# Optimization experiments

Measured on AMD Instinct MI355X. Metric: run time of the kernel, lower is better.

The kernel has to match this reference:

```python
import jax, jax.numpy as jnp
import numpy as np

N = 50000      # nodes
E = 400000     # edges (before self-loops)
F_IN = 128     # input_embedding_dim
HID = 256      # hidden_dim
HEADS = 4      # gat_heads
C1 = HID // HEADS  # per-head channels layer 0
OUT = 128      # output_node_dim
G = 64         # graphs in batch
NEG_SLOPE = 0.2


def setup_inputs() -> dict:
    key = jax.random.key(0)
    ks = jax.random.split(key, 12)
    s = lambda fan: 1.0 / np.sqrt(fan)
    embedded_x = jax.random.normal(ks[0], (N, F_IN), jnp.float32)
    edge_index = jax.random.randint(ks[1], (2, E), 0, N, dtype=jnp.int32)
    batch_idx = jnp.sort(jax.random.randint(ks[2], (N,), 0, G, dtype=jnp.int32))
    # layer 0: GATConv(F_IN -> C1, heads=HEADS, concat=True)
    W1 = jax.random.normal(ks[3], (F_IN, HEADS * C1), jnp.float32) * s(F_IN)
    att_src1 = jax.random.normal(ks[4], (HEADS, C1), jnp.float32) * s(C1)
    att_dst1 = jax.random.normal(ks[5], (HEADS, C1), jnp.float32) * s(C1)
    b1 = jnp.zeros((HEADS * C1,), jnp.float32)
    # layer 1 (last): GATConv(HID -> OUT, heads=1, concat=False)
    W2 = jax.random.normal(ks[6], (HID, OUT), jnp.float32) * s(HID)
    att_src2 = jax.random.normal(ks[7], (1, OUT), jnp.float32) * s(OUT)
    att_dst2 = jax.random.normal(ks[8], (1, OUT), jnp.float32) * s(OUT)
    b2 = jnp.zeros((OUT,), jnp.float32)
    return {"embedded_x": embedded_x, "edge_index": edge_index, "batch_idx": batch_idx,
            "W1": W1, "att_src1": att_src1, "att_dst1": att_dst1, "b1": b1,
            "W2": W2, "att_src2": att_src2, "att_dst2": att_dst2, "b2": b2}


def gat_conv(x, src, dst, W, att_src, att_dst, bias, heads, out_ch, concat):
    n = x.shape[0]
    xw = (x @ W).reshape(n, heads, out_ch)              # [N,H,C]
    a_s = (xw * att_src[None]).sum(-1)                  # [N,H]
    a_d = (xw * att_dst[None]).sum(-1)                  # [N,H]
    e = jax.nn.leaky_relu(a_s[src] + a_d[dst], NEG_SLOPE)  # [E',H]
    # segment softmax over incoming edges of each dst node (self-loops guarantee non-empty)
    m = jax.ops.segment_max(e, dst, num_segments=n)
    ee = jnp.exp(e - m[dst])
    denom = jax.ops.segment_sum(ee, dst, num_segments=n)
    alpha = ee / denom[dst]                             # [E',H]
    msg = xw[src] * alpha[:, :, None]                   # [E',H,C]
    out = jax.ops.segment_sum(msg, dst, num_segments=n) # [N,H,C]
    out = out.reshape(n, heads * out_ch) if concat else out.mean(axis=1)
    return out + bias


def reference(embedded_x, edge_index, batch_idx, W1, att_src1, att_dst1, b1, W2, att_src2, att_dst2, b2):
    loops = jnp.arange(N, dtype=edge_index.dtype)
    src = jnp.concatenate([edge_index[0], loops])
    dst = jnp.concatenate([edge_index[1], loops])
    h = gat_conv(embedded_x, src, dst, W1, att_src1, att_dst1, b1, HEADS, C1, True)
    h = jax.nn.elu(h)  # dropout is identity in eval
    h = gat_conv(h, src, dst, W2, att_src2, att_dst2, b2, 1, OUT, False)
    h = jax.nn.elu(h)
    # final_node_transform is Identity (current_dim == output_node_dim)
    counts = jax.ops.segment_sum(jnp.ones((N,), h.dtype), batch_idx, num_segments=G)
    graph_embedding = jax.ops.segment_sum(h, batch_idx, num_segments=G) / jnp.maximum(counts, 1.0)[:, None]
    return (graph_embedding, h)
```

## Files before the change

kernel.cpp:

```cpp
#include <hip/hip_runtime.h>

#define NN   50000
#define NE   400000
#define NET  450000
#define NG   64
#define NEG  0.2f

using bf16x8 = __attribute__((ext_vector_type(8))) short;
using f32x4  = __attribute__((ext_vector_type(4))) float;

__device__ inline float b2f(unsigned short u){
  union{unsigned int i; float f;} v; v.i = ((unsigned int)u) << 16; return v.f;
}
__device__ inline unsigned short f2b(float f){
  union{float f; unsigned int i;} v; v.f = f;
  unsigned int r = (v.i + 0x7fffu + ((v.i >> 16) & 1u)) >> 16;
  return (unsigned short)r;
}
__device__ inline float sane(float o){
  return (o > -1e30f && o < 1e30f) ? o : 0.f;
}
__device__ inline float lrelu_clamp(float e){
  e = fmaxf(e, NEG * e);
  return fminf(e, 60.f);
}

__global__ void zero_all(int* __restrict__ deg, float* __restrict__ pools, int* __restrict__ cnt){
  int i = blockIdx.x * 256 + threadIdx.x;
  if (i < NN) deg[i] = 0;
  if (i < NG * 128) pools[i] = 0.f;
  if (i < NG) cnt[i] = 0;
}

__device__ inline void pack_one(const float* W, unsigned short* Bp, int t, int K, int N){
  int nk = K / 32;
  int lane = t & 63; int rest = t >> 6;
  int kit = rest % nk; int nt = rest / nk;
  int quad = lane >> 4, n = lane & 15;
  unsigned short* dst = Bp + (size_t)t * 8;
#pragma unroll
  for (int j = 0; j < 8; j++)
    dst[j] = f2b(W[(size_t)(kit*32 + quad*8 + j) * N + nt*16 + n]);
}
__global__ void pack_both(const float* __restrict__ W1, const float* __restrict__ W2,
                          unsigned short* __restrict__ Bp1, unsigned short* __restrict__ Bp2){
  int t = blockIdx.x * 256 + threadIdx.x;
  if (t < 4096) pack_one(W1, Bp1, t, 128, 256);
  else          pack_one(W2, Bp2, t - 4096, 256, 128);
}

__global__ void gemm1_fused(const float* __restrict__ X, const unsigned short* __restrict__ Bp,
                            const float* __restrict__ av, const float* __restrict__ dv,
                            unsigned short* __restrict__ C,
                            float* __restrict__ a_s, float* __restrict__ a_d){
  constexpr int NK = 4, NT = 16;
  int lane = threadIdx.x & 63, wave = threadIdx.x >> 6;
  int mbase = (blockIdx.x * 4 + wave) * 16;
  if (mbase >= NN) return;
  int quad = lane >> 4, nn = lane & 15;
  int arow = mbase + nn; if (arow >= NN) arow = NN - 1;
  const float* Xr = X + (size_t)arow * 128 + quad * 8;
  bf16x8 afrag[NK];
#pragma unroll
  for (int kit = 0; kit < NK; kit++){
    bf16x8 a;
#pragma unroll
    for (int j = 0; j < 8; j++) a[j] = (short)f2b(Xr[kit * 32 + j]);
    afrag[kit] = a;
  }
  float sd0=0,sd1=0,sd2=0,sd3=0, dd0=0,dd1=0,dd2=0,dd3=0;
#pragma unroll
  for (int nt = 0; nt < NT; nt++){
    f32x4 acc = {0.f, 0.f, 0.f, 0.f};
#pragma unroll
    for (int kit = 0; kit < NK; kit++){
      bf16x8 bfrag = *(const bf16x8*)(Bp + ((size_t)(nt*NK + kit) * 64 + lane) * 8);
      acc = __builtin_amdgcn_mfma_f32_16x16x32_bf16(afrag[kit], bfrag, acc, 0, 0, 0);
    }
    int col = nt * 16 + nn;
    float avc = av[col], dvc = dv[col];
    sd0 += acc[0]*avc; dd0 += acc[0]*dvc;
    sd1 += acc[1]*avc; dd1 += acc[1]*dvc;
    sd2 += acc[2]*avc; dd2 += acc[2]*dvc;
    sd3 += acc[3]*avc; dd3 += acc[3]*dvc;
#pragma unroll
    for (int r = 0; r < 4; r++){
      int row = mbase + quad * 4 + r;
      if (row < NN) C[(size_t)row * 256 + col] = f2b(acc[r]);
    }
    if ((nt & 3) == 3){
      int hh = nt >> 2;
#pragma unroll
      for (int off = 1; off < 16; off <<= 1){
        sd0 += __shfl_xor(sd0, off); sd1 += __shfl_xor(sd1, off);
        sd2 += __shfl_xor(sd2, off); sd3 += __shfl_xor(sd3, off);
        dd0 += __shfl_xor(dd0, off); dd1 += __shfl_xor(dd1, off);
        dd2 += __shfl_xor(dd2, off); dd3 += __shfl_xor(dd3, off);
      }
      if (nn == 0){
        int row = mbase + quad * 4;
        if (row + 0 < NN){ a_s[(row+0)*4+hh] = sd0; a_d[(row+0)*4+hh] = dd0; }
        if (row + 1 < NN){ a_s[(row+1)*4+hh] = sd1; a_d[(row+1)*4+hh] = dd1; }
        if (row + 2 < NN){ a_s[(row+2)*4+hh] = sd2; a_d[(row+2)*4+hh] = dd2; }
        if (row + 3 < NN){ a_s[(row+3)*4+hh] = sd3; a_d[(row+3)*4+hh] = dd3; }
      }
      sd0=sd1=sd2=sd3=dd0=dd1=dd2=dd3=0.f;
    }
  }
}

__global__ void gemm2_fused(const unsigned short* __restrict__ A, const unsigned short* __restrict__ Bp,
                            const float* __restrict__ av, const float* __restrict__ dv,
                            unsigned short* __restrict__ C,
                            float* __restrict__ a_s, float* __restrict__ a_d){
  constexpr int NK = 8, NT = 8;
  int lane = threadIdx.x & 63, wave = threadIdx.x >> 6;
  int mbase = (blockIdx.x * 4 + wave) * 16;
  if (mbase >= NN) return;
  int quad = lane >> 4, nn = lane & 15;
  int arow = mbase + nn; if (arow >= NN) arow = NN - 1;
  const unsigned short* Ar = A + (size_t)arow * 256 + quad * 8;
  bf16x8 afrag[NK];
#pragma unroll
  for (int kit = 0; kit < NK; kit++)
    afrag[kit] = *(const bf16x8*)(Ar + kit * 32);
  float sd0=0,sd1=0,sd2=0,sd3=0, dd0=0,dd1=0,dd2=0,dd3=0;
#pragma unroll
  for (int nt = 0; nt < NT; nt++){
    f32x4 acc = {0.f, 0.f, 0.f, 0.f};
#pragma unroll
    for (int kit = 0; kit < NK; kit++){
      bf16x8 bfrag = *(const bf16x8*)(Bp + ((size_t)(nt*NK + kit) * 64 + lane) * 8);
      acc = __builtin_amdgcn_mfma_f32_16x16x32_bf16(afrag[kit], bfrag, acc, 0, 0, 0);
    }
    int col = nt * 16 + nn;
    float avc = av[col], dvc = dv[col];
    sd0 += acc[0]*avc; dd0 += acc[0]*dvc;
    sd1 += acc[1]*avc; dd1 += acc[1]*dvc;
    sd2 += acc[2]*avc; dd2 += acc[2]*dvc;
    sd3 += acc[3]*avc; dd3 += acc[3]*dvc;
#pragma unroll
    for (int r = 0; r < 4; r++){
      int row = mbase + quad * 4 + r;
      if (row < NN) C[(size_t)row * 128 + col] = f2b(acc[r]);
    }
  }
#pragma unroll
  for (int off = 1; off < 16; off <<= 1){
    sd0 += __shfl_xor(sd0, off); sd1 += __shfl_xor(sd1, off);
    sd2 += __shfl_xor(sd2, off); sd3 += __shfl_xor(sd3, off);
    dd0 += __shfl_xor(dd0, off); dd1 += __shfl_xor(dd1, off);
    dd2 += __shfl_xor(dd2, off); dd3 += __shfl_xor(dd3, off);
  }
  if (nn == 0){
    int row = mbase + quad * 4;
    if (row + 0 < NN){ a_s[row+0] = sd0; a_d[row+0] = dd0; }
    if (row + 1 < NN){ a_s[row+1] = sd1; a_d[row+1] = dd1; }
    if (row + 2 < NN){ a_s[row+2] = sd2; a_d[row+2] = dd2; }
    if (row + 3 < NN){ a_s[row+3] = sd3; a_d[row+3] = dd3; }
  }
}

__global__ void count_deg(const int* __restrict__ ei, int* __restrict__ deg){
  int t = blockIdx.x * blockDim.x + threadIdx.x;
  if (t >= NET) return;
  int d = (t < NE) ? ei[NE + t] : (t - NE);
  if (d < 0) d = 0; if (d >= NN) d = NN - 1;
  atomicAdd(&deg[d], 1);
}

__global__ void scan_block(const int* __restrict__ in, int* __restrict__ out_excl,
                           int* __restrict__ bsums, int n){
  __shared__ int s[256];
  int tid = threadIdx.x, gid = blockIdx.x * 256 + tid;
  int v = (gid < n) ? in[gid] : 0;
  s[tid] = v; __syncthreads();
  for (int off = 1; off < 256; off <<= 1){
    int t = (tid >= off) ? s[tid - off] : 0;
    __syncthreads();
    s[tid] += t;
    __syncthreads();
  }
  if (gid < n) out_excl[gid] = s[tid] - v;
  if (tid == 255) bsums[blockIdx.x] = s[255];
}

__global__ void scan_add2(int* __restrict__ offs, const int* __restrict__ bsums,
                          int* __restrict__ cursor, int n){
  __shared__ int lds[256];
  int b = blockIdx.x, tid = threadIdx.x;
  int v = 0;
  for (int i = tid; i < b; i += 256) v += bsums[i];
  lds[tid] = v; __syncthreads();
  for (int off = 128; off; off >>= 1){
    if (tid < off) lds[tid] += lds[tid + off];
    __syncthreads();
  }
  int prefix = lds[0];
  int gid = b * 256 + tid;
  if (gid < n){
    int o = offs[gid] + prefix;
    offs[gid] = o; cursor[gid] = o;
  }
  if (gid == 0) offs[n] = NET;
}

__global__ void fill_csr(const int* __restrict__ ei, int* __restrict__ cursor,
                         int* __restrict__ csr){
  int t = blockIdx.x * blockDim.x + threadIdx.x;
  if (t >= NET) return;
  int s = (t < NE) ? ei[t]      : (t - NE);
  int d = (t < NE) ? ei[NE + t] : (t - NE);
  if (d < 0) d = 0; if (d >= NN) d = NN - 1;
  int pos = atomicAdd(&cursor[d], 1);
  if (pos >= 0 && pos < NET) csr[pos] = s;
}

__global__ void agg1(const unsigned short* __restrict__ xw, const float* __restrict__ a_s,
                     const float* __restrict__ a_d, const int* __restrict__ offs,
                     const int* __restrict__ csr, const float* __restrict__ bias,
                     unsigned short* __restrict__ h1){
  int lane = threadIdx.x & 63;
  int node = (blockIdx.x * blockDim.x + threadIdx.x) >> 6;
  if (node >= NN) return;
  int h = lane >> 4;
  int beg = offs[node], end = offs[node + 1];
  if (beg < 0) beg = 0; if (end > NET) end = NET;
  float adv = a_d[node * 4 + h];
  float l0=0,l1=0,l2=0,l3=0;
  float c00=0,c01=0,c02=0,c03=0;
  float c10=0,c11=0,c12=0,c13=0;
  float c20=0,c21=0,c22=0,c23=0;
  float c30=0,c31=0,c32=0,c33=0;
  int e = beg;
  for (; e + 8 <= end; e += 8){
    int s0 = csr[e],   s1 = csr[e+1], s2 = csr[e+2], s3 = csr[e+3];
    int s4 = csr[e+4], s5 = csr[e+5], s6 = csr[e+6], s7 = csr[e+7];
    float p0 = __expf(lrelu_clamp(a_s[s0*4+h] + adv));
    float p1 = __expf(lrelu_clamp(a_s[s1*4+h] + adv));
    float p2 = __expf(lrelu_clamp(a_s[s2*4+h] + adv));
    float p3 = __expf(lrelu_clamp(a_s[s3*4+h] + adv));
    float p4 = __expf(lrelu_clamp(a_s[s4*4+h] + adv));
    float p5 = __expf(lrelu_clamp(a_s[s5*4+h] + adv));
    float p6 = __expf(lrelu_clamp(a_s[s6*4+h] + adv));
    float p7 = __expf(lrelu_clamp(a_s[s7*4+h] + adv));
    ushort4 x0 = *(const ushort4*)(xw + (size_t)s0 * 256 + lane * 4);
    ushort4 x1 = *(const ushort4*)(xw + (size_t)s1 * 256 + lane * 4);
    ushort4 x2 = *(const ushort4*)(xw + (size_t)s2 * 256 + lane * 4);
    ushort4 x3 = *(const ushort4*)(xw + (size_t)s3 * 256 + lane * 4);
    ushort4 x4 = *(const ushort4*)(xw + (size_t)s4 * 256 + lane * 4);
    ushort4 x5 = *(const ushort4*)(xw + (size_t)s5 * 256 + lane * 4);
    ushort4 x6 = *(const ushort4*)(xw + (size_t)s6 * 256 + lane * 4);
    ushort4 x7 = *(const ushort4*)(xw + (size_t)s7 * 256 + lane * 4);
    l0 += p0 + p4; l1 += p1 + p5; l2 += p2 + p6; l3 += p3 + p7;
    c00 += p0*b2f(x0.x); c01 += p0*b2f(x0.y); c02 += p0*b2f(x0.z); c03 += p0*b2f(x0.w);
    c10 += p1*b2f(x1.x); c11 += p1*b2f(x1.y); c12 += p1*b2f(x1.z); c13 += p1*b2f(x1.w);
    c20 += p2*b2f(x2.x); c21 += p2*b2f(x2.y); c22 += p2*b2f(x2.z); c23 += p2*b2f(x2.w);
    c30 += p3*b2f(x3.x); c31 += p3*b2f(x3.y); c32 += p3*b2f(x3.z); c33 += p3*b2f(x3.w);
    c00 += p4*b2f(x4.x); c01 += p4*b2f(x4.y); c02 += p4*b2f(x4.z); c03 += p4*b2f(x4.w);
    c10 += p5*b2f(x5.x); c11 += p5*b2f(x5.y); c12 += p5*b2f(x5.z); c13 += p5*b2f(x5.w);
    c20 += p6*b2f(x6.x); c21 += p6*b2f(x6.y); c22 += p6*b2f(x6.z); c23 += p6*b2f(x6.w);
    c30 += p7*b2f(x7.x); c31 += p7*b2f(x7.y); c32 += p7*b2f(x7.z); c33 += p7*b2f(x7.w);
  }
  for (; e < end; e++){
    int s0 = csr[e];
    float p0 = __expf(lrelu_clamp(a_s[s0*4+h] + adv));
    ushort4 x0 = *(const ushort4*)(xw + (size_t)s0 * 256 + lane * 4);
    l0 += p0; c00 += p0*b2f(x0.x); c01 += p0*b2f(x0.y); c02 += p0*b2f(x0.z); c03 += p0*b2f(x0.w);
  }
  float l = (l0 + l1) + (l2 + l3);
  float C0 = (c00 + c10) + (c20 + c30);
  float C1 = (c01 + c11) + (c21 + c31);
  float C2 = (c02 + c12) + (c22 + c32);
  float C3 = (c03 + c13) + (c23 + c33);
  if (!(l > 0.f)) l = 1.f;
  float inv = 1.f / l;
  float4 b4 = *(const float4*)(bias + lane * 4);
  float v; ushort4 o;
  v = C0 * inv + b4.x; v = v > 0.f ? v : expm1f(v); o.x = f2b(sane(v));
  v = C1 * inv + b4.y; v = v > 0.f ? v : expm1f(v); o.y = f2b(sane(v));
  v = C2 * inv + b4.z; v = v > 0.f ? v : expm1f(v); o.z = f2b(sane(v));
  v = C3 * inv + b4.w; v = v > 0.f ? v : expm1f(v); o.w = f2b(sane(v));
  *(ushort4*)(h1 + (size_t)node * 256 + lane * 4) = o;
}

__global__ void agg2(const unsigned short* __restrict__ xw, const float* __restrict__ a_s,
                     const float* __restrict__ a_d, const int* __restrict__ offs,
                     const int* __restrict__ csr, const float* __restrict__ bias,
                     float* __restrict__ hout){
  int lane = threadIdx.x & 63;
  int node = (blockIdx.x * blockDim.x + threadIdx.x) >> 6;
  if (node >= NN) return;
  int beg = offs[node], end = offs[node + 1];
  if (beg < 0) beg = 0; if (end > NET) end = NET;
  float adv = a_d[node];
  float l0=0,l1=0,l2=0,l3=0;
  float c00=0,c01=0, c10=0,c11=0, c20=0,c21=0, c30=0,c31=0;
  int e = beg;
  for (; e + 8 <= end; e += 8){
    int s0 = csr[e],   s1 = csr[e+1], s2 = csr[e+2], s3 = csr[e+3];
    int s4 = csr[e+4], s5 = csr[e+5], s6 = csr[e+6], s7 = csr[e+7];
    float p0 = __expf(lrelu_clamp(a_s[s0] + adv));
    float p1 = __expf(lrelu_clamp(a_s[s1] + adv));
    float p2 = __expf(lrelu_clamp(a_s[s2] + adv));
    float p3 = __expf(lrelu_clamp(a_s[s3] + adv));
    float p4 = __expf(lrelu_clamp(a_s[s4] + adv));
    float p5 = __expf(lrelu_clamp(a_s[s5] + adv));
    float p6 = __expf(lrelu_clamp(a_s[s6] + adv));
    float p7 = __expf(lrelu_clamp(a_s[s7] + adv));
    ushort2 x0 = *(const ushort2*)(xw + (size_t)s0 * 128 + lane * 2);
    ushort2 x1 = *(const ushort2*)(xw + (size_t)s1 * 128 + lane * 2);
    ushort2 x2 = *(const ushort2*)(xw + (size_t)s2 * 128 + lane * 2);
    ushort2 x3 = *(const ushort2*)(xw + (size_t)s3 * 128 + lane * 2);
    ushort2 x4 = *(const ushort2*)(xw + (size_t)s4 * 128 + lane * 2);
    ushort2 x5 = *(const ushort2*)(xw + (size_t)s5 * 128 + lane * 2);
    ushort2 x6 = *(const ushort2*)(xw + (size_t)s6 * 128 + lane * 2);
    ushort2 x7 = *(const ushort2*)(xw + (size_t)s7 * 128 + lane * 2);
    l0 += p0 + p4; l1 += p1 + p5; l2 += p2 + p6; l3 += p3 + p7;
    c00 += p0*b2f(x0.x); c01 += p0*b2f(x0.y);
    c10 += p1*b2f(x1.x); c11 += p1*b2f(x1.y);
    c20 += p2*b2f(x2.x); c21 += p2*b2f(x2.y);
    c30 += p3*b2f(x3.x); c31 += p3*b2f(x3.y);
    c00 += p4*b2f(x4.x); c01 += p4*b2f(x4.y);
    c10 += p5*b2f(x5.x); c11 += p5*b2f(x5.y);
    c20 += p6*b2f(x6.x); c21 += p6*b2f(x6.y);
    c30 += p7*b2f(x7.x); c31 += p7*b2f(x7.y);
  }
  for (; e < end; e++){
    int s0 = csr[e];
    float p0 = __expf(lrelu_clamp(a_s[s0] + adv));
    ushort2 x0 = *(const ushort2*)(xw + (size_t)s0 * 128 + lane * 2);
    l0 += p0; c00 += p0*b2f(x0.x); c01 += p0*b2f(x0.y);
  }
  float l = (l0 + l1) + (l2 + l3);
  float C0 = (c00 + c10) + (c20 + c30);
  float C1 = (c01 + c11) + (c21 + c31);
  if (!(l > 0.f)) l = 1.f;
  float inv = 1.f / l;
  float v0 = C0 * inv + bias[lane*2];   v0 = v0 > 0.f ? v0 : expm1f(v0);
  float v1 = C1 * inv + bias[lane*2+1]; v1 = v1 > 0.f ? v1 : expm1f(v1);
  float2 o; o.x = sane(v0); o.y = sane(v1);
  *(float2*)(hout + (size_t)node * 128 + lane * 2) = o;
}

__global__ void pool_kernel(const float* __restrict__ h, const int* __restrict__ batch,
                            float* __restrict__ pools, int* __restrict__ cnt){
  int c = threadIdx.x;
  int n0 = blockIdx.x * 16;
  if (n0 >= NN) return;
  int nend = n0 + 16; if (nend > NN) nend = NN;
  int cur = batch[n0];
  cur = (cur < 0) ? 0 : (cur >= NG ? NG - 1 : cur);
  float sum = 0.f; int count = 0;
  for (int n = n0; n < nend; n++){
    int g = batch[n];
    g = (g < 0) ? 0 : (g >= NG ? NG - 1 : g);
    if (g != cur){
      atomicAdd(&pools[cur * 128 + c], sum);
      if (c == 0) atomicAdd(&cnt[cur], count);
      sum = 0.f; count = 0; cur = g;
    }
    sum += h[(size_t)n * 128 + c];
    count++;
  }
  atomicAdd(&pools[cur * 128 + c], sum);
  if (c == 0) atomicAdd(&cnt[cur], count);
}

__global__ void final_kernel(const float* __restrict__ pools, const int* __restrict__ cnt,
                             float* __restrict__ out){
  int g = blockIdx.x, c = threadIdx.x;
  float d = fmaxf((float)cnt[g], 1.0f);
  out[g * 128 + c] = sane(pools[g * 128 + c] / d);
}

extern "C" void kernel_launch(void* const* d_in, const int* in_sizes, int n_in,
                              void* d_out, int out_size, void* d_ws, size_t ws_size,
                              hipStream_t stream){
  const float* x    = (const float*)d_in[0];
  const int*   ei   = (const int*)d_in[1];
  const int*   bat  = (const int*)d_in[2];
  const float* W1   = (const float*)d_in[3];
  const float* av1  = (const float*)d_in[4];
  const float* dv1  = (const float*)d_in[5];
  const float* b1   = (const float*)d_in[6];
  const float* W2   = (const float*)d_in[7];
  const float* av2  = (const float*)d_in[8];
  const float* dv2  = (const float*)d_in[9];
  const float* b2   = (const float*)d_in[10];

  char* w = (char*)d_ws;
  size_t o = 0;
  auto carve = [&](size_t bytes) -> char* {
    char* p = w + o; o += (bytes + 255) & ~(size_t)255; return p;
  };
  unsigned short* Bp1   = (unsigned short*)carve((size_t)4096 * 8 * 2);
  unsigned short* Bp2   = (unsigned short*)carve((size_t)4096 * 8 * 2);
  float*          a_s1v = (float*)carve((size_t)NN * 4 * 4);
  float*          a_d1v = (float*)carve((size_t)NN * 4 * 4);
  float*          a_s2v = (float*)carve((size_t)NN * 4);
  float*          a_d2v = (float*)carve((size_t)NN * 4);
  int*            deg   = (int*)carve((size_t)NN * 4);
  int*            offs  = (int*)carve((size_t)(NN + 1) * 4);
  int*            cursor= (int*)carve((size_t)NN * 4);
  int*            bsums = (int*)carve(256 * 4);
  int*            csr   = (int*)carve((size_t)NET * 4);
  float*          pools = (float*)carve((size_t)NG * 128 * 4);
  int*            cnt   = (int*)carve((size_t)NG * 4);
  unsigned short* xw1   = (unsigned short*)carve((size_t)NN * 256 * 2);
  unsigned short* h1b   = (unsigned short*)carve((size_t)NN * 256 * 2);
  unsigned short* xw2   = (unsigned short*)carve((size_t)NN * 128 * 2);

  float* out_ge = (float*)d_out;
  float* out_h  = (float*)d_out + NG * 128;

  zero_all<<<196, 256, 0, stream>>>(deg, pools, cnt);
  pack_both<<<32, 256, 0, stream>>>(W1, W2, Bp1, Bp2);

  count_deg<<<(NET + 255) / 256, 256, 0, stream>>>(ei, deg);
  scan_block<<<196, 256, 0, stream>>>(deg, offs, bsums, NN);
  scan_add2<<<196, 256, 0, stream>>>(offs, bsums, cursor, NN);
  fill_csr<<<(NET + 255) / 256, 256, 0, stream>>>(ei, cursor, csr);

  gemm1_fused<<<782, 256, 0, stream>>>(x, Bp1, av1, dv1, xw1, a_s1v, a_d1v);
  agg1<<<12500, 256, 0, stream>>>(xw1, a_s1v, a_d1v, offs, csr, b1, h1b);

  gemm2_fused<<<782, 256, 0, stream>>>(h1b, Bp2, av2, dv2, xw2, a_s2v, a_d2v);
  agg2<<<12500, 256, 0, stream>>>(xw2, a_s2v, a_d2v, offs, csr, b2, out_h);

  pool_kernel<<<3125, 128, 0, stream>>>(out_h, bat, pools, cnt);
  final_kernel<<<NG, 128, 0, stream>>>(pools, cnt, out_ge);
}
```

Measured before the change: 286.2 us.

## Precompute per-edge attention weights in separate edge passes before aggregation

Adds edge-parallel kernels that compute exp(leaky_relu(a_s+a_d)) once per edge and head, scattering them into CSR order using positions recorded by fill_csr. The aggregation kernels then read these weights instead of recomputing the exp for every lane, and their unroll drops from 8 to 4. The intent is to cut redundant transcendental work and scattered a_s gathers inside the wave-per-node loops. The cost is two extra launches and extra global traffic for the weight arrays, and xw2 now reuses xw1's buffer.

```diff
diff --git a/kernel.cpp b/kernel.cpp
--- a/kernel.cpp
+++ b/kernel.cpp
@@ -206,65 +206,83 @@
 }
 
 __global__ void fill_csr(const int* __restrict__ ei, int* __restrict__ cursor,
-                         int* __restrict__ csr){
+                         int* __restrict__ csr, int* __restrict__ epos){
   int t = blockIdx.x * blockDim.x + threadIdx.x;
   if (t >= NET) return;
   int s = (t < NE) ? ei[t]      : (t - NE);
   int d = (t < NE) ? ei[NE + t] : (t - NE);
   if (d < 0) d = 0; if (d >= NN) d = NN - 1;
   int pos = atomicAdd(&cursor[d], 1);
-  if (pos >= 0 && pos < NET) csr[pos] = s;
-}
-
-__global__ void agg1(const unsigned short* __restrict__ xw, const float* __restrict__ a_s,
-                     const float* __restrict__ a_d, const int* __restrict__ offs,
-                     const int* __restrict__ csr, const float* __restrict__ bias,
-                     unsigned short* __restrict__ h1){
+  if (pos < 0) pos = 0; if (pos >= NET) pos = NET - 1;
+  csr[pos] = s;
+  epos[t] = pos;
+}
+
+__global__ void epass1(const int* __restrict__ ei, const int* __restrict__ epos,
+                       const float* __restrict__ a_s, const float* __restrict__ a_d,
+                       float* __restrict__ pw){
+  int t = blockIdx.x * 256 + threadIdx.x;
+  if (t >= NET) return;
+  int s = (t < NE) ? ei[t]      : (t - NE);
+  int d = (t < NE) ? ei[NE + t] : (t - NE);
+  if (s < 0) s = 0; if (s >= NN) s = NN - 1;
+  if (d < 0) d = 0; if (d >= NN) d = NN - 1;
+  int pos = epos[t];
+  float4 as = *(const float4*)(a_s + (size_t)s * 4);
+  float4 ad = *(const float4*)(a_d + (size_t)d * 4);
+  float4 p;
+  p.x = __expf(lrelu_clamp(as.x + ad.x));
+  p.y = __expf(lrelu_clamp(as.y + ad.y));
+  p.z = __expf(lrelu_clamp(as.z + ad.z));
+  p.w = __expf(lrelu_clamp(as.w + ad.w));
+  *(float4*)(pw + (size_t)pos * 4) = p;
+}
+
+__global__ void epass2(const int* __restrict__ ei, const int* __restrict__ epos,
+                       const float* __restrict__ a_s, const float* __restrict__ a_d,
+                       float* __restrict__ pw){
+  int t = blockIdx.x * 256 + threadIdx.x;
+  if (t >= NET) return;
+  int s = (t < NE) ? ei[t]      : (t - NE);
+  int d = (t < NE) ? ei[NE + t] : (t - NE);
+  if (s < 0) s = 0; if (s >= NN) s = NN - 1;
+  if (d < 0) d = 0; if (d >= NN) d = NN - 1;
+  pw[epos[t]] = __expf(lrelu_clamp(a_s[s] + a_d[d]));
+}
+
+__global__ void agg1(const unsigned short* __restrict__ xw, const float* __restrict__ pw,
+                     const int* __restrict__ offs, const int* __restrict__ csr,
+                     const float* __restrict__ bias, unsigned short* __restrict__ h1){
   int lane = threadIdx.x & 63;
   int node = (blockIdx.x * blockDim.x + threadIdx.x) >> 6;
   if (node >= NN) return;
   int h = lane >> 4;
   int beg = offs[node], end = offs[node + 1];
   if (beg < 0) beg = 0; if (end > NET) end = NET;
-  float adv = a_d[node * 4 + h];
   float l0=0,l1=0,l2=0,l3=0;
   float c00=0,c01=0,c02=0,c03=0;
   float c10=0,c11=0,c12=0,c13=0;
   float c20=0,c21=0,c22=0,c23=0;
   float c30=0,c31=0,c32=0,c33=0;
   int e = beg;
-  for (; e + 8 <= end; e += 8){
-    int s0 = csr[e],   s1 = csr[e+1], s2 = csr[e+2], s3 = csr[e+3];
-    int s4 = csr[e+4], s5 = csr[e+5], s6 = csr[e+6], s7 = csr[e+7];
-    float p0 = __expf(lrelu_clamp(a_s[s0*4+h] + adv));
-    float p1 = __expf(lrelu_clamp(a_s[s1*4+h] + adv));
-    float p2 = __expf(lrelu_clamp(a_s[s2*4+h] + adv));
-    float p3 = __expf(lrelu_clamp(a_s[s3*4+h] + adv));
-    float p4 = __expf(lrelu_clamp(a_s[s4*4+h] + adv));
-    float p5 = __expf(lrelu_clamp(a_s[s5*4+h] + adv));
-    float p6 = __expf(lrelu_clamp(a_s[s6*4+h] + adv));
-    float p7 = __expf(lrelu_clamp(a_s[s7*4+h] + adv));
+  for (; e + 4 <= end; e += 4){
+    int s0 = csr[e], s1 = csr[e+1], s2 = csr[e+2], s3 = csr[e+3];
+    float p0 = pw[(size_t)(e+0)*4 + h];
+    float p1 = pw[(size_t)(e+1)*4 + h];
+    float p2 = pw[(size_t)(e+2)*4 + h];
+    float p3 = pw[(size_t)(e+3)*4 + h];
     ushort4 x0 = *(const ushort4*)(xw + (size_t)s0 * 256 + lane * 4);
     ushort4 x1 = *(const ushort4*)(xw + (size_t)s1 * 256 + lane * 4);
     ushort4 x2 = *(const ushort4*)(xw + (size_t)s2 * 256 + lane * 4);
     ushort4 x3 = *(const ushort4*)(xw + (size_t)s3 * 256 + lane * 4);
-    ushort4 x4 = *(const ushort4*)(xw + (size_t)s4 * 256 + lane * 4);
-    ushort4 x5 = *(const ushort4*)(xw + (size_t)s5 * 256 + lane * 4);
-    ushort4 x6 = *(const ushort4*)(xw + (size_t)s6 * 256 + lane * 4);
-    ushort4 x7 = *(const ushort4*)(xw + (size_t)s7 * 256 + lane * 4);
-    l0 += p0 + p4; l1 += p1 + p5; l2 += p2 + p6; l3 += p3 + p7;
-    c00 += p0*b2f(x0.x); c01 += p0*b2f(x0.y); c02 += p0*b2f(x0.z); c03 += p0*b2f(x0.w);
-    c10 += p1*b2f(x1.x); c11 += p1*b2f(x1.y); c12 += p1*b2f(x1.z); c13 += p1*b2f(x1.w);
-    c20 += p2*b2f(x2.x); c21 += p2*b2f(x2.y); c22 += p2*b2f(x2.z); c23 += p2*b2f(x2.w);
-    c30 += p3*b2f(x3.x); c31 += p3*b2f(x3.y); c32 += p3*b2f(x3.z); c33 += p3*b2f(x3.w);
-    c00 += p4*b2f(x4.x); c01 += p4*b2f(x4.y); c02 += p4*b2f(x4.z); c03 += p4*b2f(x4.w);
-    c10 += p5*b2f(x5.x); c11 += p5*b2f(x5.y); c12 += p5*b2f(x5.z); c13 += p5*b2f(x5.w);
-    c20 += p6*b2f(x6.x); c21 += p6*b2f(x6.y); c22 += p6*b2f(x6.z); c23 += p6*b2f(x6.w);
-    c30 += p7*b2f(x7.x); c31 += p7*b2f(x7.y); c32 += p7*b2f(x7.z); c33 += p7*b2f(x7.w);
+    l0 += p0; c00 += p0*b2f(x0.x); c01 += p0*b2f(x0.y); c02 += p0*b2f(x0.z); c03 += p0*b2f(x0.w);
+    l1 += p1; c10 += p1*b2f(x1.x); c11 += p1*b2f(x1.y); c12 += p1*b2f(x1.z); c13 += p1*b2f(x1.w);
+    l2 += p2; c20 += p2*b2f(x2.x); c21 += p2*b2f(x2.y); c22 += p2*b2f(x2.z); c23 += p2*b2f(x2.w);
+    l3 += p3; c30 += p3*b2f(x3.x); c31 += p3*b2f(x3.y); c32 += p3*b2f(x3.z); c33 += p3*b2f(x3.w);
   }
   for (; e < end; e++){
     int s0 = csr[e];
-    float p0 = __expf(lrelu_clamp(a_s[s0*4+h] + adv));
+    float p0 = pw[(size_t)e*4 + h];
     ushort4 x0 = *(const ushort4*)(xw + (size_t)s0 * 256 + lane * 4);
     l0 += p0; c00 += p0*b2f(x0.x); c01 += p0*b2f(x0.y); c02 += p0*b2f(x0.z); c03 += p0*b2f(x0.w);
   }
@@ -284,51 +302,32 @@
   *(ushort4*)(h1 + (size_t)node * 256 + lane * 4) = o;
 }
 
-__global__ void agg2(const unsigned short* __restrict__ xw, const float* __restrict__ a_s,
-                     const float* __restrict__ a_d, const int* __restrict__ offs,
-                     const int* __restrict__ csr, const float* __restrict__ bias,
-                     float* __restrict__ hout){
+__global__ void agg2(const unsigned short* __restrict__ xw, const float* __restrict__ pw,
+                     const int* __restrict__ offs, const int* __restrict__ csr,
+                     const float* __restrict__ bias, float* __restrict__ hout){
   int lane = threadIdx.x & 63;
   int node = (blockIdx.x * blockDim.x + threadIdx.x) >> 6;
   if (node >= NN) return;
   int beg = offs[node], end = offs[node + 1];
   if (beg < 0) beg = 0; if (end > NET) end = NET;
-  float adv = a_d[node];
   float l0=0,l1=0,l2=0,l3=0;
   float c00=0,c01=0, c10=0,c11=0, c20=0,c21=0, c30=0,c31=0;
   int e = beg;
-  for (; e + 8 <= end; e += 8){
-    int s0 = csr[e],   s1 = csr[e+1], s2 = csr[e+2], s3 = csr[e+3];
-    int s4 = csr[e+4], s5 = csr[e+5], s6 = csr[e+6], s7 = csr[e+7];
-    float p0 = __expf(lrelu_clamp(a_s[s0] + adv));
-    float p1 = __expf(lrelu_clamp(a_s[s1] + adv));
-    float p2 = __expf(lrelu_clamp(a_s[s2] + adv));
-    float p3 = __expf(lrelu_clamp(a_s[s3] + adv));
-    float p4 = __expf(lrelu_clamp(a_s[s4] + adv));
-    float p5 = __expf(lrelu_clamp(a_s[s5] + adv));
-    float p6 = __expf(lrelu_clamp(a_s[s6] + adv));
-    float p7 = __expf(lrelu_clamp(a_s[s7] + adv));
+  for (; e + 4 <= end; e += 4){
+    int s0 = csr[e], s1 = csr[e+1], s2 = csr[e+2], s3 = csr[e+3];
+    float p0 = pw[e+0], p1 = pw[e+1], p2 = pw[e+2], p3 = pw[e+3];
     ushort2 x0 = *(const ushort2*)(xw + (size_t)s0 * 128 + lane * 2);
     ushort2 x1 = *(const ushort2*)(xw + (size_t)s1 * 128 + lane * 2);
     ushort2 x2 = *(const ushort2*)(xw + (size_t)s2 * 128 + lane * 2);
     ushort2 x3 = *(const ushort2*)(xw + (size_t)s3 * 128 + lane * 2);
-    ushort2 x4 = *(const ushort2*)(xw + (size_t)s4 * 128 + lane * 2);
-    ushort2 x5 = *(const ushort2*)(xw + (size_t)s5 * 128 + lane * 2);
-    ushort2 x6 = *(const ushort2*)(xw + (size_t)s6 * 128 + lane * 2);
-    ushort2 x7 = *(const ushort2*)(xw + (size_t)s7 * 128 + lane * 2);
-    l0 += p0 + p4; l1 += p1 + p5; l2 += p2 + p6; l3 += p3 + p7;
-    c00 += p0*b2f(x0.x); c01 += p0*b2f(x0.y);
-    c10 += p1*b2f(x1.x); c11 += p1*b2f(x1.y);
-    c20 += p2*b2f(x2.x); c21 += p2*b2f(x2.y);
-    c30 += p3*b2f(x3.x); c31 += p3*b2f(x3.y);
-    c00 += p4*b2f(x4.x); c01 += p4*b2f(x4.y);
-    c10 += p5*b2f(x5.x); c11 += p5*b2f(x5.y);
-    c20 += p6*b2f(x6.x); c21 += p6*b2f(x6.y);
-    c30 += p7*b2f(x7.x); c31 += p7*b2f(x7.y);
+    l0 += p0; c00 += p0*b2f(x0.x); c01 += p0*b2f(x0.y);
+    l1 += p1; c10 += p1*b2f(x1.x); c11 += p1*b2f(x1.y);
+    l2 += p2; c20 += p2*b2f(x2.x); c21 += p2*b2f(x2.y);
+    l3 += p3; c30 += p3*b2f(x3.x); c31 += p3*b2f(x3.y);
   }
   for (; e < end; e++){
     int s0 = csr[e];
-    float p0 = __expf(lrelu_clamp(a_s[s0] + adv));
+    float p0 = pw[e];
     ushort2 x0 = *(const ushort2*)(xw + (size_t)s0 * 128 + lane * 2);
     l0 += p0; c00 += p0*b2f(x0.x); c01 += p0*b2f(x0.y);
   }
@@ -405,11 +404,14 @@
   int*            cursor= (int*)carve((size_t)NN * 4);
   int*            bsums = (int*)carve(256 * 4);
   int*            csr   = (int*)carve((size_t)NET * 4);
+  int*            epos  = (int*)carve((size_t)NET * 4);
+  float*          pw1   = (float*)carve((size_t)NET * 4 * 4);
+  float*          pw2   = (float*)carve((size_t)NET * 4);
   float*          pools = (float*)carve((size_t)NG * 128 * 4);
   int*            cnt   = (int*)carve((size_t)NG * 4);
   unsigned short* xw1   = (unsigned short*)carve((size_t)NN * 256 * 2);
   unsigned short* h1b   = (unsigned short*)carve((size_t)NN * 256 * 2);
-  unsigned short* xw2   = (unsigned short*)carve((size_t)NN * 128 * 2);
+  unsigned short* xw2   = xw1;
 
   float* out_ge = (float*)d_out;
   float* out_h  = (float*)d_out + NG * 128;
@@ -420,13 +422,15 @@
   count_deg<<<(NET + 255) / 256, 256, 0, stream>>>(ei, deg);
   scan_block<<<196, 256, 0, stream>>>(deg, offs, bsums, NN);
   scan_add2<<<196, 256, 0, stream>>>(offs, bsums, cursor, NN);
-  fill_csr<<<(NET + 255) / 256, 256, 0, stream>>>(ei, cursor, csr);
+  fill_csr<<<(NET + 255) / 256, 256, 0, stream>>>(ei, cursor, csr, epos);
 
   gemm1_fused<<<782, 256, 0, stream>>>(x, Bp1, av1, dv1, xw1, a_s1v, a_d1v);
-  agg1<<<12500, 256, 0, stream>>>(xw1, a_s1v, a_d1v, offs, csr, b1, h1b);
+  epass1<<<(NET + 255) / 256, 256, 0, stream>>>(ei, epos, a_s1v, a_d1v, pw1);
+  agg1<<<12500, 256, 0, stream>>>(xw1, pw1, offs, csr, b1, h1b);
 
   gemm2_fused<<<782, 256, 0, stream>>>(h1b, Bp2, av2, dv2, xw2, a_s2v, a_d2v);
-  agg2<<<12500, 256, 0, stream>>>(xw2, a_s2v, a_d2v, offs, csr, b2, out_h);
+  epass2<<<(NET + 255) / 256, 256, 0, stream>>>(ei, epos, a_s2v, a_d2v, pw2);
+  agg2<<<12500, 256, 0, stream>>>(xw2, pw2, offs, csr, b2, out_h);
 
   pool_kernel<<<3125, 128, 0, stream>>>(out_h, bat, pools, cnt);
   final_kernel<<<NG, 128, 0, stream>>>(pools, cnt, out_ge);
```

Result: no change. 290.3 us (+1.4%).
